# Kernel optimization log

Measured on AMD Instinct MI355X. Metric: run time of the kernel, lower is better.

## Reference

```python
import jax, jax.numpy as jnp
import numpy as np

N_ITERS = 100   # fixed ADMM (OSQP-style) iteration count
RHO = 1.0       # ADMM penalty
SIGMA = 1e-6    # OSQP regularization


def setup_inputs() -> dict:
    key = jax.random.key(0)
    ks = jax.random.split(key, 12)
    B, S, H, nA = 16384, 512, 1024, 24
    mEq, mIneq = 4, 8
    state = jax.random.normal(ks[0], (B, S), dtype=jnp.float32)
    Aeq = jax.random.normal(ks[1], (mEq, nA), dtype=jnp.float32)
    beq = jax.random.normal(ks[2], (mEq,), dtype=jnp.float32)
    A = jax.random.normal(ks[3], (mIneq, nA), dtype=jnp.float32)
    b = jax.random.uniform(ks[4], (mIneq,), dtype=jnp.float32)
    ub = jnp.ones((nA,), dtype=jnp.float32)
    lb = jnp.zeros((nA,), dtype=jnp.float32)
    # MLP parameters (3 Dense layers as in the flax module)
    W1 = jax.random.normal(ks[5], (S, H), dtype=jnp.float32) / np.sqrt(S).astype(np.float32)
    b1 = jnp.zeros((H,), dtype=jnp.float32)
    W2 = jax.random.normal(ks[6], (H, H), dtype=jnp.float32) / np.sqrt(H).astype(np.float32)
    b2 = jnp.zeros((H,), dtype=jnp.float32)
    W3 = jax.random.normal(ks[7], (H, nA), dtype=jnp.float32) / np.sqrt(H).astype(np.float32)
    b3 = jnp.zeros((nA,), dtype=jnp.float32)
    return dict(state=state, Aeq=Aeq, beq=beq, A=A, b=b, ub=ub, lb=lb,
                W1=W1, b1=b1, W2=W2, b2=b2, W3=W3, b3=b3)


def reference(state, Aeq, beq, A, b, ub, lb, W1, b1, W2, b2, W3, b3):
    # ---- 3-layer MLP ----
    h = jax.nn.relu(state @ W1 + b1)
    h = jax.nn.relu(h @ W2 + b2)
    raw = h @ W3 + b3                      # [B, n]
    n = raw.shape[-1]
    I = jnp.eye(n, dtype=raw.dtype)
    # ---- stack constraints exactly as solve_qp: [Aeq; A_ineq; I; -I] ----
    A_tot = jnp.concatenate([Aeq, A, I, -I], axis=0)            # [M, n]
    neg_inf = jnp.full((A.shape[0],), -jnp.inf, dtype=raw.dtype)
    l_tot = jnp.concatenate([beq, neg_inf, lb, -ub])            # [M]
    u_tot = jnp.concatenate([beq, b, ub, -lb])                  # [M]
    # ---- OSQP-style ADMM: min 0.5||x||^2 - raw'x  s.t. l <= A_tot x <= u ----
    q = -raw                                                    # [B, n]
    M = (1.0 + SIGMA) * I + RHO * (A_tot.T @ A_tot)             # [n, n] (P = I)
    Minv = jnp.linalg.inv(M)
    B_, m = q.shape[0], A_tot.shape[0]
    X0 = jnp.zeros_like(q)
    Z0 = jnp.zeros((B_, m), dtype=q.dtype)
    Y0 = jnp.zeros((B_, m), dtype=q.dtype)

    def step(carry, _):
        X, Z, Y = carry
        rhs = SIGMA * X - q + (RHO * Z - Y) @ A_tot             # [B, n]
        Xn = rhs @ Minv.T                                       # [B, n]
        Zt = Xn @ A_tot.T                                       # [B, m]
        Zn = jnp.clip(Zt + Y / RHO, l_tot, u_tot)
        Yn = Y + RHO * (Zt - Zn)
        return (Xn, Zn, Yn), None

    (X, Z, Y), _ = jax.lax.scan(step, (X0, Z0, Y0), None, length=N_ITERS)
    return X
```

## Files before the change

### kernel.cpp

```cpp
#include <hip/hip_runtime.h>

using uint = unsigned int;
using ushort = unsigned short;

typedef __attribute__((ext_vector_type(8))) short bf16x8;
typedef __attribute__((ext_vector_type(4))) float f32x4;

#define ADMM_ITERS 100
#define RHO_C 1.0f
#define SIGMA_C 1e-6f

__device__ inline ushort f2bf(float f) {
  union { float f; uint u; } c; c.f = f;
  uint u = c.u;
  uint r = (u + 0x7fffu + ((u >> 16) & 1u)) >> 16;
  return (ushort)r;
}

__device__ inline void gload_lds16(const void* g, void* l) {
  __builtin_amdgcn_global_load_lds(
      (const __attribute__((address_space(1))) void*)g,
      (__attribute__((address_space(3))) void*)l, 16, 0, 0);
}

__device__ inline void splitPack(const float* x, bf16x8& hi, bf16x8& lo) {
#pragma unroll
  for (int j = 0; j < 8; ++j) {
    uint b = __float_as_uint(x[j]);
    uint hb = b & 0xffff0000u;
    float lf = x[j] - __uint_as_float(hb);
    hi[j] = (short)(b >> 16);
    lo[j] = (short)(__float_as_uint(lf) >> 16);
  }
}

__global__ void convert_bf16(const float* __restrict__ in, ushort* __restrict__ out, int n4) {
  int i = blockIdx.x * blockDim.x + threadIdx.x;
  if (i >= n4) return;
  float4 v = ((const float4*)in)[i];
  uint2 p;
  p.x = (uint)f2bf(v.x) | ((uint)f2bf(v.y) << 16);
  p.y = (uint)f2bf(v.z) | ((uint)f2bf(v.w) << 16);
  ((uint2*)out)[i] = p;
}

__global__ void transpose_f32_bf16(const float* __restrict__ in, ushort* __restrict__ out,
                                   int R, int C, int Cout) {
  __shared__ float t[32][33];
  const int c0 = blockIdx.x * 32, r0 = blockIdx.y * 32;
  const int tx = threadIdx.x & 31, ty = threadIdx.x >> 5;
  for (int rr = ty; rr < 32; rr += 8) {
    int r = r0 + rr, c = c0 + tx;
    float v = 0.0f;
    if (r < R && c < C) v = in[(long)r * C + c];
    t[rr][tx] = v;
  }
  __syncthreads();
  for (int rr = ty; rr < 32; rr += 8) {
    int c = c0 + rr, r = r0 + tx;
    if (c < Cout && r < R) out[(long)c * R + r] = f2bf(t[tx][rr]);
  }
}

__global__ void setup_admm(const float* __restrict__ Aeq, const float* __restrict__ beq,
                           const float* __restrict__ A, const float* __restrict__ b,
                           const float* __restrict__ ub, const float* __restrict__ lb,
                           ushort* __restrict__ Th, ushort* __restrict__ Tl,
                           ushort* __restrict__ T0h, ushort* __restrict__ T0l,
                           float* __restrict__ blp, float* __restrict__ bup) {
  __shared__ float Aug[24][48];
  __shared__ float A12[12 * 24];
  __shared__ float fac[24];
  __shared__ float Tx[24][36];
  const int t = threadIdx.x;
  for (int i = t; i < 48 * 64; i += 256) { Th[i] = 0; Tl[i] = 0; }
  for (int i = t; i < 48 * 32; i += 256) { T0h[i] = 0; T0l[i] = 0; }
  if (t < 96)  A12[t] = Aeq[t];
  if (t < 192) A12[96 + t] = A[t];
  __syncthreads();
  for (int idx = t; idx < 576; idx += 256) {
    int j = idx / 24, k = idx % 24;
    float s = (j == k) ? (1.0f + SIGMA_C + 2.0f * RHO_C) : 0.0f;
    for (int r = 0; r < 12; ++r) s += RHO_C * A12[r * 24 + j] * A12[r * 24 + k];
    Aug[j][k] = s;
    Aug[j][24 + k] = (j == k) ? 1.0f : 0.0f;
  }
  __syncthreads();
  for (int p = 0; p < 24; ++p) {
    float rp = 1.0f / Aug[p][p];
    if (t < 24) fac[t] = Aug[t][p];
    __syncthreads();
    if (t < 48) Aug[p][t] *= rp;
    __syncthreads();
    for (int idx = t; idx < 24 * 48; idx += 256) {
      int r = idx / 48, c = idx % 48;
      if (r != p) Aug[r][c] -= fac[r] * Aug[p][c];
    }
    __syncthreads();
  }
  auto splitStore = [](ushort* hp, ushort* lp, int i, float v) {
    ushort hs = f2bf(v);
    float hf = __uint_as_float(((uint)hs) << 16);
    ushort ls = f2bf(v - hf);
    hp[i] = hs; lp[i] = ls;
  };
  for (int idx = t; idx < 24 * 36; idx += 256) {
    int n = idx / 36, k = idx % 36;
    float v;
    if (k < 24) v = 2.0f * Aug[n][24 + k];
    else {
      v = 0.0f;
      for (int j = 0; j < 24; ++j) v += Aug[n][24 + j] * A12[(k - 24) * 24 + j];
    }
    Tx[n][k] = v;
    splitStore(Th, Tl, n * 64 + k, v);
  }
  __syncthreads();
  for (int idx = t; idx < 12 * 36; idx += 256) {
    int m = idx / 36, k = idx % 36;
    float v = 0.0f;
    for (int j = 0; j < 24; ++j) v += A12[m * 24 + j] * Tx[j][k];
    splitStore(Th, Tl, (24 + m) * 64 + k, v);
  }
  for (int idx = t; idx < 36 * 24; idx += 256) {
    int n = idx / 24, k = idx % 24;
    float v;
    if (n < 24) v = Aug[n][24 + k];
    else {
      v = 0.0f;
      for (int j = 0; j < 24; ++j) v += A12[(n - 24) * 24 + j] * Aug[j][24 + k];
    }
    splitStore(T0h, T0l, n * 32 + k, v);
  }
  if (t < 48) {
    float lv, uv;
    if (t < 24)      { lv = lb[t]; uv = ub[t]; }
    else if (t < 28) { lv = beq[t - 24]; uv = lv; }
    else if (t < 36) { lv = -1e30f; uv = b[t - 28]; }
    else             { lv = -1e30f; uv = 1e30f; }
    blp[t] = lv; bup[t] = uv;
  }
}

template<int BM, int BN, int WM, int WN, int TM, int TN, int MODE>
__global__ __launch_bounds__(256) void gemm_bt(
    const ushort* __restrict__ A, const ushort* __restrict__ Bt,
    const float* __restrict__ bias, void* __restrict__ Cout_,
    int K, int ldc, int nvalid) {
  __shared__ char lds[(BM + BN) * 64];
  char* ldsA = lds;
  char* ldsB = lds + BM * 64;

  const int tid = threadIdx.x;
  const int wave = tid >> 6;
  const int lane = tid & 63;
  const int blockM = blockIdx.y * BM;
  const int blockN = blockIdx.x * BN;
  const int wm = (wave / WN) * (TM * 16);
  const int wn = (wave % WN) * (TN * 16);

  f32x4 acc[TM][TN] = {};

  const int l15 = lane & 15;
  const int kq = lane >> 4;
  constexpr int AI = BM / 16;
  constexpr int TOT = (BM + BN) / 16;
  const int srow = lane >> 2;
  const int kb = (lane & 3) ^ ((srow >> 1) & 3);

  for (int k0 = 0; k0 < K; k0 += 32) {
    for (int inst = wave; inst < TOT; inst += 4) {
      const bool isA = inst < AI;
      const int i = isA ? inst : inst - AI;
      const ushort* gp = (isA ? A : Bt)
          + (long)((isA ? blockM : blockN) + i * 16 + srow) * K + (k0 + kb * 8);
      char* lp = (isA ? ldsA : ldsB) + i * 1024;
      gload_lds16(gp, lp);
    }
    __syncthreads();

    bf16x8 af[TM], bfr[TN];
#pragma unroll
    for (int i = 0; i < TM; ++i) {
      int r = wm + i * 16 + l15;
      int ch = kq ^ ((r >> 1) & 3);
      af[i] = *(const bf16x8*)(ldsA + r * 64 + ch * 16);
    }
#pragma unroll
    for (int j = 0; j < TN; ++j) {
      int r = wn + j * 16 + l15;
      int ch = kq ^ ((r >> 1) & 3);
      bfr[j] = *(const bf16x8*)(ldsB + r * 64 + ch * 16);
    }
#pragma unroll
    for (int i = 0; i < TM; ++i)
#pragma unroll
      for (int j = 0; j < TN; ++j)
        acc[i][j] = __builtin_amdgcn_mfma_f32_16x16x32_bf16(af[i], bfr[j], acc[i][j], 0, 0, 0);
    __syncthreads();
  }

  const int ro = lane >> 4;
#pragma unroll
  for (int i = 0; i < TM; ++i) {
#pragma unroll
    for (int j = 0; j < TN; ++j) {
      const int col = blockN + wn + j * 16 + l15;
      float bv;
      if (MODE == 0) bv = bias[col];
      else bv = (col < nvalid) ? bias[col] : 0.0f;
#pragma unroll
      for (int r = 0; r < 4; ++r) {
        const int row = blockM + wm + i * 16 + ro * 4 + r;
        float v = acc[i][j][r] + bv;
        if (MODE == 0) {
          v = fmaxf(v, 0.0f);
          ((ushort*)Cout_)[(long)row * ldc + col] = f2bf(v);
        } else {
          if (col < nvalid) ((float*)Cout_)[(long)row * ldc + col] = v;
        }
      }
    }
  }
}

#define GEMM8P_QUAD(MI0, NJ0)                                                 \
  _Pragma("unroll") for (int mi_ = 0; mi_ < 4; ++mi_)                         \
  _Pragma("unroll") for (int nj_ = 0; nj_ < 2; ++nj_)                         \
  _Pragma("unroll") for (int kk_ = 0; kk_ < 2; ++kk_)                         \
    acc[(MI0) + mi_][(NJ0) + nj_] = __builtin_amdgcn_mfma_f32_16x16x32_bf16(  \
        aF[mi_][kk_], bF[(NJ0) + nj_][kk_], acc[(MI0) + mi_][(NJ0) + nj_],    \
        0, 0, 0);

#define GEMM8P_SYNC_PRE()                              \
  __builtin_amdgcn_s_barrier();                        \
  asm volatile("s_waitcnt lgkmcnt(0)" ::: "memory");   \
  __builtin_amdgcn_sched_barrier(0);                   \
  __builtin_amdgcn_s_setprio(1);

#define GEMM8P_SYNC_POST()                             \
  __builtin_amdgcn_s_setprio(0);                       \
  __builtin_amdgcn_s_barrier();

__global__ __launch_bounds__(512, 2) void gemm8p(
    const ushort* __restrict__ A, const ushort* __restrict__ Bt,
    const float* __restrict__ bias, ushort* __restrict__ Cout,
    int K, int ldc, int nblk_n) {
  __shared__ __align__(16) char ldsc[131072];

  const int nwg = gridDim.x;
  const int bid = blockIdx.x;
  const int swz = (bid & 7) * (nwg >> 3) + (bid >> 3);
  const int blockM = (swz / nblk_n) * 256;
  const int blockN = (swz % nblk_n) * 256;

  const int tid = threadIdx.x;
  const int wave = tid >> 6;
  const int lane = tid & 63;
  const int l15 = lane & 15;
  const int q = lane >> 4;
  const int wm = (wave >> 2) * 128;
  const int wn = (wave & 3) * 64;
  const int nt = K >> 6;

  f32x4 acc[8][4] = {};

  auto stage = [&](int ts, int h) {
    if (ts >= nt) return;
    char* base = ldsc + ((ts & 1) << 16) + (h << 14);
#pragma unroll
    for (int j = 0; j < 2; ++j) {
      const int idx = wave * 64 + j * 512 + lane;
      const int row = idx >> 3;
      const int cs = (idx & 7) ^ (row & 7);
      const ushort* gp =
          (h < 2 ? A + (long)(blockM + ((h & 1) << 7) + row) * K
                 : Bt + (long)(blockN + ((h & 1) << 7) + row) * K)
          + (ts << 6) + cs * 8;
      gload_lds16(gp, base + ((wave * 64 + j * 512) << 4));
    }
  };
  auto dsA = [&](int cb, int mi, int kk) {
    const int r = wm + mi * 16 + l15;
    const int cs = (kk * 4 + q) ^ (r & 7);
    return *(const bf16x8*)(ldsc + (cb << 16) + r * 128 + cs * 16);
  };
  auto dsB = [&](int cb, int nj, int kk) {
    const int r = wn + nj * 16 + l15;
    const int cs = (kk * 4 + q) ^ (r & 7);
    return *(const bf16x8*)(ldsc + (cb << 16) + 32768 + r * 128 + cs * 16);
  };

  stage(0, 0); stage(0, 1); stage(0, 2); stage(0, 3);
  stage(1, 0);
  asm volatile("s_waitcnt vmcnt(2)" ::: "memory");
  __builtin_amdgcn_s_barrier();

  bf16x8 aF[4][2], bF[4][2];
#pragma unroll 1
  for (int t = 0; t < nt; ++t) {
    const int cb = t & 1;
#pragma unroll
    for (int mi = 0; mi < 4; ++mi)
#pragma unroll
      for (int kk = 0; kk < 2; ++kk) aF[mi][kk] = dsA(cb, mi, kk);
#pragma unroll
    for (int nj = 0; nj < 2; ++nj)
#pragma unroll
      for (int kk = 0; kk < 2; ++kk) bF[nj][kk] = dsB(cb, nj, kk);
    stage(t + 1, 1);
    GEMM8P_SYNC_PRE();
    GEMM8P_QUAD(0, 0);
    GEMM8P_SYNC_POST();
#pragma unroll
    for (int nj = 2; nj < 4; ++nj)
#pragma unroll
      for (int kk = 0; kk < 2; ++kk) bF[nj][kk] = dsB(cb, nj, kk);
    stage(t + 1, 2);
    GEMM8P_SYNC_PRE();
    GEMM8P_QUAD(0, 2);
    GEMM8P_SYNC_POST();
#pragma unroll
    for (int mi = 0; mi < 4; ++mi)
#pragma unroll
      for (int kk = 0; kk < 2; ++kk) aF[mi][kk] = dsA(cb, 4 + mi, kk);
    stage(t + 1, 3);
    GEMM8P_SYNC_PRE();
    GEMM8P_QUAD(4, 2);
    GEMM8P_SYNC_POST();
    stage(t + 2, 0);
    if (t + 2 < nt) { asm volatile("s_waitcnt vmcnt(2)" ::: "memory"); }
    else            { asm volatile("s_waitcnt vmcnt(0)" ::: "memory"); }
    __builtin_amdgcn_s_barrier();
    __builtin_amdgcn_s_setprio(1);
    GEMM8P_QUAD(4, 0);
    GEMM8P_SYNC_POST();
  }

#pragma unroll
  for (int mi = 0; mi < 8; ++mi) {
#pragma unroll
    for (int nj = 0; nj < 4; ++nj) {
      const int col = blockN + wn + nj * 16 + l15;
      const float bv = bias[col];
#pragma unroll
      for (int r = 0; r < 4; ++r) {
        const int row = blockM + wm + mi * 16 + q * 4 + r;
        float v = acc[mi][nj][r] + bv;
        v = fmaxf(v, 0.0f);
        Cout[(long)row * ldc + col] = f2bf(v);
      }
    }
  }
}

__global__ __launch_bounds__(256) void admm_mfma(
    const float* raw,
    const ushort* __restrict__ Th, const ushort* __restrict__ Tl,
    const ushort* __restrict__ T0h, const ushort* __restrict__ T0l,
    const float* __restrict__ blp, const float* __restrict__ bup,
    float* outp) {
  __shared__ __align__(16) float Ubuf[4][16][68];
  const int tid = threadIdx.x, wave = tid >> 6, lane = tid & 63;
  const int l15 = lane & 15, q = lane >> 4;
  const long rowbase = (long)blockIdx.x * 64 + wave * 16;
  float (*U)[68] = Ubuf[wave];

  for (int idx = lane; idx < 256; idx += 64)
    U[idx >> 4][48 + (idx & 15)] = 0.0f;

  float bl[3], bu[3];
#pragma unroll
  for (int t = 0; t < 3; ++t) { bl[t] = blp[16 * t + l15]; bu[t] = bup[16 * t + l15]; }

  f32x4 W[3], base[3];
  {
    bf16x8 t0h[3], t0l[3];
#pragma unroll
    for (int t = 0; t < 3; ++t) {
      t0h[t] = *(const bf16x8*)(T0h + (16 * t + l15) * 32 + q * 8);
      t0l[t] = *(const bf16x8*)(T0l + (16 * t + l15) * 32 + q * 8);
    }
    float qa[8];
    if (q < 3) {
      const float* rp = raw + (rowbase + l15) * 24 + q * 8;
      float4 v0 = *(const float4*)rp;
      float4 v1 = *(const float4*)(rp + 4);
      qa[0] = v0.x; qa[1] = v0.y; qa[2] = v0.z; qa[3] = v0.w;
      qa[4] = v1.x; qa[5] = v1.y; qa[6] = v1.z; qa[7] = v1.w;
    } else {
#pragma unroll
      for (int j = 0; j < 8; ++j) qa[j] = 0.0f;
    }
    bf16x8 qhi, qlo;
    splitPack(qa, qhi, qlo);
#pragma unroll
    for (int t = 0; t < 3; ++t) {
      f32x4 acc = {0.0f, 0.0f, 0.0f, 0.0f};
      acc = __builtin_amdgcn_mfma_f32_16x16x32_bf16(qhi, t0h[t], acc, 0, 0, 0);
      acc = __builtin_amdgcn_mfma_f32_16x16x32_bf16(qlo, t0h[t], acc, 0, 0, 0);
      acc = __builtin_amdgcn_mfma_f32_16x16x32_bf16(qhi, t0l[t], acc, 0, 0, 0);
      base[t] = acc; W[t] = acc;
    }
  }

  bf16x8 tbh[2][3], tbl[2][3];
#pragma unroll
  for (int c = 0; c < 2; ++c)
#pragma unroll
    for (int t = 0; t < 3; ++t) {
      tbh[c][t] = *(const bf16x8*)(Th + (16 * t + l15) * 64 + 32 * c + q * 8);
      tbl[c][t] = *(const bf16x8*)(Tl + (16 * t + l15) * 64 + 32 * c + q * 8);
    }

  float yb0[4], yb1[4];
#pragma unroll 1
  for (int it = 1; it < ADMM_ITERS; ++it) {
    f32x4 C[3];
#pragma unroll
    for (int t = 0; t < 3; ++t) {
#pragma unroll
      for (int r = 0; r < 4; ++r) {
        float w = W[t][r];
        float z = fminf(fmaxf(w, bl[t]), bu[t]);
        float u = 2.0f * z - w;
        float y = w - z;
        C[t][r] = base[t][r] + y;
        if (t == 0) yb0[r] = y;
        if (t == 1) yb1[r] = y;
        U[q * 4 + r][16 * t + l15] = u;
      }
    }
    bf16x8 uh[2], ul[2];
#pragma unroll
    for (int c = 0; c < 2; ++c) {
      const float* up = &U[l15][32 * c + q * 8];
      float4 a0 = *(const float4*)up;
      float4 a1 = *(const float4*)(up + 4);
      float ua[8] = {a0.x, a0.y, a0.z, a0.w, a1.x, a1.y, a1.z, a1.w};
      splitPack(ua, uh[c], ul[c]);
    }
#pragma unroll
    for (int t = 0; t < 3; ++t) {
      f32x4 acc = C[t];
#pragma unroll
      for (int c = 0; c < 2; ++c) {
        acc = __builtin_amdgcn_mfma_f32_16x16x32_bf16(uh[c], tbh[c][t], acc, 0, 0, 0);
        acc = __builtin_amdgcn_mfma_f32_16x16x32_bf16(ul[c], tbh[c][t], acc, 0, 0, 0);
        acc = __builtin_amdgcn_mfma_f32_16x16x32_bf16(uh[c], tbl[c][t], acc, 0, 0, 0);
      }
      W[t] = acc;
    }
  }

#pragma unroll
  for (int r = 0; r < 4; ++r) {
    const long row = rowbase + q * 4 + r;
    outp[row * 24 + l15] = W[0][r] - yb0[r];
    if (l15 < 8) outp[row * 24 + 16 + l15] = W[1][r] - yb1[r];
  }
}

extern "C" void kernel_launch(void* const* d_in, const int* in_sizes, int n_in,
                              void* d_out, int out_size, void* d_ws, size_t ws_size,
                              hipStream_t stream) {
  const float* state = (const float*)d_in[0];
  const float* Aeq   = (const float*)d_in[1];
  const float* beq   = (const float*)d_in[2];
  const float* Ain   = (const float*)d_in[3];
  const float* bin   = (const float*)d_in[4];
  const float* ub    = (const float*)d_in[5];
  const float* lb    = (const float*)d_in[6];
  const float* W1    = (const float*)d_in[7];
  const float* b1    = (const float*)d_in[8];
  const float* W2    = (const float*)d_in[9];
  const float* b2    = (const float*)d_in[10];
  const float* W3    = (const float*)d_in[11];
  const float* b3    = (const float*)d_in[12];

  const int Bn = in_sizes[0] / 512;
  char* ws = (char*)d_ws;
  ushort* stateB = (ushort*)(ws + 0);
  ushort* W1T    = (ushort*)(ws + 16777216);
  ushort* W2T    = (ushort*)(ws + 17825792);
  ushort* W3T    = (ushort*)(ws + 19922944);
  ushort* Th     = (ushort*)(ws + 19993600);
  ushort* Tl     = (ushort*)(ws + 19999744);
  ushort* T0h    = (ushort*)(ws + 20005888);
  ushort* T0l    = (ushort*)(ws + 20008960);
  float*  blp    = (float*) (ws + 20012032);
  float*  bup    = (float*) (ws + 20012224);
  ushort* H1     = (ushort*)(ws + 21565440);
  ushort* H2     = (ushort*)(ws + 55119872);
  float*  rawb   = (float*)d_out;

  const int n4 = (Bn * 512) / 4;
  convert_bf16<<<(n4 + 255) / 256, 256, 0, stream>>>(state, stateB, n4);
  transpose_f32_bf16<<<dim3(32, 16), 256, 0, stream>>>(W1, W1T, 512, 1024, 1024);
  transpose_f32_bf16<<<dim3(32, 32), 256, 0, stream>>>(W2, W2T, 1024, 1024, 1024);
  transpose_f32_bf16<<<dim3(1, 32),  256, 0, stream>>>(W3, W3T, 1024, 24, 32);
  setup_admm<<<1, 256, 0, stream>>>(Aeq, beq, Ain, bin, ub, lb,
                                    Th, Tl, T0h, T0l, blp, bup);

  const int nblkN = 1024 / 256;
  const int nwg = (Bn / 256) * nblkN;
  gemm8p<<<nwg, 512, 0, stream>>>(stateB, W1T, b1, H1, 512, 1024, nblkN);
  gemm8p<<<nwg, 512, 0, stream>>>(H1, W2T, b2, H2, 1024, 1024, nblkN);
  gemm_bt<64, 32, 4, 1, 1, 2, 1><<<dim3(1, Bn / 64), 256, 0, stream>>>(
      H2, W3T, b3, rawb, 1024, 24, 24);

  admm_mfma<<<Bn / 64, 256, 0, stream>>>(rawb, Th, Tl, T0h, T0l, blp, bup,
                                         (float*)d_out);
}
```

Measured before the change: 259.3 us.

## Merge prep kernels into one launch and drop LDS round-trip in ADMM loop

Five setup kernels (state convert, three weight transposes, ADMM setup) are combined into a single prep_all launch that dispatches on block index, removing per-launch overhead and serialization gaps. The ADMM kernel swaps MFMA operand roles so the output layout matches the input layout, which removes the per-iteration LDS scatter and gather. It uses 16x16x16 bf16 MFMAs with three independent accumulators in place of the 16x16x32 chain. The output is written with vector stores. This relies on the computation being correct when Aeq/bounds are loaded per q, and it adds more MFMA instructions per iteration.

```diff
diff --git a/kernel.cpp b/kernel.cpp
--- a/kernel.cpp
+++ b/kernel.cpp
@@ -4,6 +4,7 @@
 using ushort = unsigned short;
 
 typedef __attribute__((ext_vector_type(8))) short bf16x8;
+typedef __attribute__((ext_vector_type(4))) short bf16x4;
 typedef __attribute__((ext_vector_type(4))) float f32x4;
 
 #define ADMM_ITERS 100
@@ -34,21 +35,21 @@
   }
 }
 
-__global__ void convert_bf16(const float* __restrict__ in, ushort* __restrict__ out, int n4) {
-  int i = blockIdx.x * blockDim.x + threadIdx.x;
-  if (i >= n4) return;
-  float4 v = ((const float4*)in)[i];
-  uint2 p;
-  p.x = (uint)f2bf(v.x) | ((uint)f2bf(v.y) << 16);
-  p.y = (uint)f2bf(v.z) | ((uint)f2bf(v.w) << 16);
-  ((uint2*)out)[i] = p;
-}
-
-__global__ void transpose_f32_bf16(const float* __restrict__ in, ushort* __restrict__ out,
-                                   int R, int C, int Cout) {
+__device__ inline void splitPack4(const f32x4& x, bf16x4& hi, bf16x4& lo) {
+#pragma unroll
+  for (int j = 0; j < 4; ++j) {
+    uint b = __float_as_uint(x[j]);
+    float lf = x[j] - __uint_as_float(b & 0xffff0000u);
+    hi[j] = (short)(b >> 16);
+    lo[j] = (short)(__float_as_uint(lf) >> 16);
+  }
+}
+
+__device__ void transpose_body(const float* __restrict__ in, ushort* __restrict__ out,
+                               int R, int C, int Cout, int bx, int by, int tid) {
   __shared__ float t[32][33];
-  const int c0 = blockIdx.x * 32, r0 = blockIdx.y * 32;
-  const int tx = threadIdx.x & 31, ty = threadIdx.x >> 5;
+  const int c0 = bx * 32, r0 = by * 32;
+  const int tx = tid & 31, ty = tid >> 5;
   for (int rr = ty; rr < 32; rr += 8) {
     int r = r0 + rr, c = c0 + tx;
     float v = 0.0f;
@@ -62,17 +63,16 @@
   }
 }
 
-__global__ void setup_admm(const float* __restrict__ Aeq, const float* __restrict__ beq,
+__device__ void setup_body(const float* __restrict__ Aeq, const float* __restrict__ beq,
                            const float* __restrict__ A, const float* __restrict__ b,
                            const float* __restrict__ ub, const float* __restrict__ lb,
                            ushort* __restrict__ Th, ushort* __restrict__ Tl,
                            ushort* __restrict__ T0h, ushort* __restrict__ T0l,
-                           float* __restrict__ blp, float* __restrict__ bup) {
+                           float* __restrict__ blp, float* __restrict__ bup, int t) {
   __shared__ float Aug[24][48];
   __shared__ float A12[12 * 24];
   __shared__ float fac[24];
   __shared__ float Tx[24][36];
-  const int t = threadIdx.x;
   for (int i = t; i < 48 * 64; i += 256) { Th[i] = 0; Tl[i] = 0; }
   for (int i = t; i < 48 * 32; i += 256) { T0h[i] = 0; T0l[i] = 0; }
   if (t < 96)  A12[t] = Aeq[t];
@@ -142,6 +142,39 @@
   }
 }
 
+__global__ void prep_all(
+    const float* __restrict__ state, ushort* __restrict__ stateB, int n4,
+    const float* __restrict__ W1, ushort* __restrict__ W1T,
+    const float* __restrict__ W2, ushort* __restrict__ W2T,
+    const float* __restrict__ W3, ushort* __restrict__ W3T,
+    const float* __restrict__ Aeq, const float* __restrict__ beq,
+    const float* __restrict__ A, const float* __restrict__ b,
+    const float* __restrict__ ub, const float* __restrict__ lb,
+    ushort* __restrict__ Th, ushort* __restrict__ Tl,
+    ushort* __restrict__ T0h, ushort* __restrict__ T0l,
+    float* __restrict__ blp, float* __restrict__ bup) {
+  const int nConv = n4 >> 8;
+  int bb = blockIdx.x;
+  if (bb < nConv) {
+    int i = bb * 256 + threadIdx.x;
+    if (i < n4) {
+      float4 v = ((const float4*)state)[i];
+      uint2 p;
+      p.x = (uint)f2bf(v.x) | ((uint)f2bf(v.y) << 16);
+      p.y = (uint)f2bf(v.z) | ((uint)f2bf(v.w) << 16);
+      ((uint2*)stateB)[i] = p;
+    }
+    return;
+  }
+  bb -= nConv;
+  if (bb < 512)  { transpose_body(W1, W1T, 512, 1024, 1024, bb & 31, bb >> 5, threadIdx.x); return; }
+  bb -= 512;
+  if (bb < 1024) { transpose_body(W2, W2T, 1024, 1024, 1024, bb & 31, bb >> 5, threadIdx.x); return; }
+  bb -= 1024;
+  if (bb < 32)   { transpose_body(W3, W3T, 1024, 24, 32, 0, bb, threadIdx.x); return; }
+  setup_body(Aeq, beq, A, b, ub, lb, Th, Tl, T0h, T0l, blp, bup, threadIdx.x);
+}
+
 template<int BM, int BN, int WM, int WN, int TM, int TN, int MODE>
 __global__ __launch_bounds__(256) void gemm_bt(
     const ushort* __restrict__ A, const ushort* __restrict__ Bt,
@@ -354,24 +387,24 @@
   }
 }
 
+#define MFMA16(a, b, c) __builtin_amdgcn_mfma_f32_16x16x16bf16_1k(a, b, c, 0, 0, 0)
+
 __global__ __launch_bounds__(256) void admm_mfma(
     const float* raw,
     const ushort* __restrict__ Th, const ushort* __restrict__ Tl,
     const ushort* __restrict__ T0h, const ushort* __restrict__ T0l,
     const float* __restrict__ blp, const float* __restrict__ bup,
     float* outp) {
-  __shared__ __align__(16) float Ubuf[4][16][68];
   const int tid = threadIdx.x, wave = tid >> 6, lane = tid & 63;
   const int l15 = lane & 15, q = lane >> 4;
   const long rowbase = (long)blockIdx.x * 64 + wave * 16;
-  float (*U)[68] = Ubuf[wave];
-
-  for (int idx = lane; idx < 256; idx += 64)
-    U[idx >> 4][48 + (idx & 15)] = 0.0f;
-
-  float bl[3], bu[3];
-#pragma unroll
-  for (int t = 0; t < 3; ++t) { bl[t] = blp[16 * t + l15]; bu[t] = bup[16 * t + l15]; }
+
+  f32x4 bl[3], bu[3];
+#pragma unroll
+  for (int t = 0; t < 3; ++t) {
+    bl[t] = *(const f32x4*)(blp + 16 * t + 4 * q);
+    bu[t] = *(const f32x4*)(bup + 16 * t + 4 * q);
+  }
 
   f32x4 W[3], base[3];
   {
@@ -397,67 +430,67 @@
 #pragma unroll
     for (int t = 0; t < 3; ++t) {
       f32x4 acc = {0.0f, 0.0f, 0.0f, 0.0f};
-      acc = __builtin_amdgcn_mfma_f32_16x16x32_bf16(qhi, t0h[t], acc, 0, 0, 0);
-      acc = __builtin_amdgcn_mfma_f32_16x16x32_bf16(qlo, t0h[t], acc, 0, 0, 0);
-      acc = __builtin_amdgcn_mfma_f32_16x16x32_bf16(qhi, t0l[t], acc, 0, 0, 0);
+      acc = __builtin_amdgcn_mfma_f32_16x16x32_bf16(t0h[t], qhi, acc, 0, 0, 0);
+      acc = __builtin_amdgcn_mfma_f32_16x16x32_bf16(t0h[t], qlo, acc, 0, 0, 0);
+      acc = __builtin_amdgcn_mfma_f32_16x16x32_bf16(t0l[t], qhi, acc, 0, 0, 0);
       base[t] = acc; W[t] = acc;
     }
   }
 
-  bf16x8 tbh[2][3], tbl[2][3];
-#pragma unroll
-  for (int c = 0; c < 2; ++c)
-#pragma unroll
-    for (int t = 0; t < 3; ++t) {
-      tbh[c][t] = *(const bf16x8*)(Th + (16 * t + l15) * 64 + 32 * c + q * 8);
-      tbl[c][t] = *(const bf16x8*)(Tl + (16 * t + l15) * 64 + 32 * c + q * 8);
-    }
-
-  float yb0[4], yb1[4];
+  bf16x4 th[3][3], tl[3][3];
+#pragma unroll
+  for (int t = 0; t < 3; ++t)
+#pragma unroll
+    for (int c = 0; c < 3; ++c) {
+      th[t][c] = *(const bf16x4*)(Th + (16 * t + l15) * 64 + 16 * c + 4 * q);
+      tl[t][c] = *(const bf16x4*)(Tl + (16 * t + l15) * 64 + 16 * c + 4 * q);
+    }
+
+  f32x4 y01[2];
 #pragma unroll 1
   for (int it = 1; it < ADMM_ITERS; ++it) {
+    bf16x4 uh[3], ul[3];
     f32x4 C[3];
 #pragma unroll
     for (int t = 0; t < 3; ++t) {
+      f32x4 u;
 #pragma unroll
       for (int r = 0; r < 4; ++r) {
         float w = W[t][r];
-        float z = fminf(fmaxf(w, bl[t]), bu[t]);
-        float u = 2.0f * z - w;
-        float y = w - z;
-        C[t][r] = base[t][r] + y;
-        if (t == 0) yb0[r] = y;
-        if (t == 1) yb1[r] = y;
-        U[q * 4 + r][16 * t + l15] = u;
+        float z = fminf(fmaxf(w, bl[t][r]), bu[t][r]);
+        float yy = w - z;
+        u[r] = z - yy;
+        C[t][r] = base[t][r] + yy;
+        if (t < 2) y01[t][r] = yy;
       }
-    }
-    bf16x8 uh[2], ul[2];
-#pragma unroll
-    for (int c = 0; c < 2; ++c) {
-      const float* up = &U[l15][32 * c + q * 8];
-      float4 a0 = *(const float4*)up;
-      float4 a1 = *(const float4*)(up + 4);
-      float ua[8] = {a0.x, a0.y, a0.z, a0.w, a1.x, a1.y, a1.z, a1.w};
-      splitPack(ua, uh[c], ul[c]);
+      splitPack4(u, uh[t], ul[t]);
     }
 #pragma unroll
     for (int t = 0; t < 3; ++t) {
-      f32x4 acc = C[t];
-#pragma unroll
-      for (int c = 0; c < 2; ++c) {
-        acc = __builtin_amdgcn_mfma_f32_16x16x32_bf16(uh[c], tbh[c][t], acc, 0, 0, 0);
-        acc = __builtin_amdgcn_mfma_f32_16x16x32_bf16(ul[c], tbh[c][t], acc, 0, 0, 0);
-        acc = __builtin_amdgcn_mfma_f32_16x16x32_bf16(uh[c], tbl[c][t], acc, 0, 0, 0);
-      }
-      W[t] = acc;
-    }
-  }
-
-#pragma unroll
-  for (int r = 0; r < 4; ++r) {
-    const long row = rowbase + q * 4 + r;
-    outp[row * 24 + l15] = W[0][r] - yb0[r];
-    if (l15 < 8) outp[row * 24 + 16 + l15] = W[1][r] - yb1[r];
+      f32x4 a0 = C[t];
+      f32x4 a1 = {0.0f, 0.0f, 0.0f, 0.0f};
+      f32x4 a2 = {0.0f, 0.0f, 0.0f, 0.0f};
+      a0 = MFMA16(th[t][0], uh[0], a0);
+      a0 = MFMA16(th[t][0], ul[0], a0);
+      a0 = MFMA16(tl[t][0], uh[0], a0);
+      a1 = MFMA16(th[t][1], uh[1], a1);
+      a1 = MFMA16(th[t][1], ul[1], a1);
+      a1 = MFMA16(tl[t][1], uh[1], a1);
+      a2 = MFMA16(th[t][2], uh[2], a2);
+      a2 = MFMA16(th[t][2], ul[2], a2);
+      a2 = MFMA16(tl[t][2], uh[2], a2);
+      W[t] = (a0 + a1) + a2;
+    }
+  }
+
+#pragma unroll
+  for (int t = 0; t < 2; ++t) {
+    if (t == 0 || q < 2) {
+      f32x4 x;
+#pragma unroll
+      for (int r = 0; r < 4; ++r) x[r] = W[t][r] - y01[t][r];
+      *(f32x4*)(outp + (rowbase + l15) * 24 + 16 * t + 4 * q) = x;
+    }
   }
 }
 
@@ -495,12 +528,11 @@
   float*  rawb   = (float*)d_out;
 
   const int n4 = (Bn * 512) / 4;
-  convert_bf16<<<(n4 + 255) / 256, 256, 0, stream>>>(state, stateB, n4);
-  transpose_f32_bf16<<<dim3(32, 16), 256, 0, stream>>>(W1, W1T, 512, 1024, 1024);
-  transpose_f32_bf16<<<dim3(32, 32), 256, 0, stream>>>(W2, W2T, 1024, 1024, 1024);
-  transpose_f32_bf16<<<dim3(1, 32),  256, 0, stream>>>(W3, W3T, 1024, 24, 32);
-  setup_admm<<<1, 256, 0, stream>>>(Aeq, beq, Ain, bin, ub, lb,
-                                    Th, Tl, T0h, T0l, blp, bup);
+  const int nConv = n4 / 256;
+  const int nPrep = nConv + 512 + 1024 + 32 + 1;
+  prep_all<<<nPrep, 256, 0, stream>>>(state, stateB, n4, W1, W1T, W2, W2T, W3, W3T,
+                                      Aeq, beq, Ain, bin, ub, lb,
+                                      Th, Tl, T0h, T0l, blp, bup);
 
   const int nblkN = 1024 / 256;
   const int nwg = (Bn / 256) * nblkN;
```

New measurement: 255.0 us. Within noise of the previous version (-1.6%).
